# Optimization experiments

Hardware: AMD Instinct MI355X
Metric: run time of the kernel (lower is better)

## Reference

```python
import jax, jax.numpy as jnp
import numpy as np

SCALE = 1.0  # args.scale


def setup_inputs() -> dict:
    key = jax.random.key(0)
    k1, k2, k3, k4, k5 = jax.random.split(key, 5)
    B, S, D, R, LR = 4, 2048, 2048, 2048, 16  # batch, seq, column(emb), row(out), lora rank
    inp = jax.random.normal(k1, (B, S, D), dtype=jnp.float32)
    weight = jax.random.normal(k2, (R, D), dtype=jnp.float32) * (1.0 / np.sqrt(D))
    bias = jax.random.normal(k3, (R,), dtype=jnp.float32)
    lora_right = jax.random.normal(k4, (B, D, LR), dtype=jnp.float32) * 0.02
    lora_left = jax.random.normal(k5, (B, LR, R), dtype=jnp.float32) * 0.02
    return {"input": inp, "weight": weight, "bias": bias,
            "lora_right": lora_right, "lora_left": lora_left}


def reference(input, weight, bias, lora_right, lora_left):
    # Base linear: x @ W^T + b  -> [B, S, R]
    x = jnp.einsum('bsd,rd->bsr', input, weight) + bias
    # Per-sample low-rank LoRA chain: (input @ right) @ left, batched
    t = jnp.einsum('bsd,bdk->bsk', input, lora_right)   # [B, S, LR]
    y = jnp.einsum('bsk,bkr->bsr', t, lora_left)        # [B, S, R]
    # L2-normalize each token vector along the last dim, then scale
    y = y / jnp.linalg.norm(y, axis=-1, keepdims=True)
    y = y * SCALE
    return x + y
```

## Files before the change

### kernel.cpp

```cpp
#include <hip/hip_runtime.h>
#include <hip/hip_bf16.h>

#define SCALE_V 1.0f

typedef __bf16 bf16v8 __attribute__((ext_vector_type(8)));
typedef float f32v4 __attribute__((ext_vector_type(4)));

typedef const __attribute__((address_space(1))) void* gas_t;
typedef __attribute__((address_space(3))) void* las_t;
#define ASYNC_COPY16(g, l) \
    __builtin_amdgcn_global_load_lds((gas_t)(g), (las_t)(l), 16, 0, 0)
#define FENCE() asm volatile("" ::: "memory")
#define MFMA __builtin_amdgcn_mfma_f32_16x16x32_bf16

__global__ __launch_bounds__(256) void transpose_lr_kernel(
    const float* __restrict__ lright, __bf16* __restrict__ lrT) {
    __shared__ float tile[16][273];
    const int b = blockIdx.y;
    const int d0 = blockIdx.x * 256;
    const int t = threadIdx.x;
    const float* src = lright + (size_t)b * 32768 + (size_t)d0 * 16;
    #pragma unroll
    for (int j = 0; j < 16; ++j) {
        tile[t & 15][j * 16 + (t >> 4)] = src[j * 256 + t];
    }
    __syncthreads();
    const int k = t >> 4, dcol = t & 15;
    __bf16* dst = lrT + (size_t)b * 32768 + (size_t)k * 2048 + d0;
    #pragma unroll
    for (int j = 0; j < 16; ++j) {
        dst[dcol + j * 16] = (__bf16)tile[k][dcol + j * 16];
    }
}

__global__ __launch_bounds__(256) void prep_kernel(
    const float* __restrict__ inp, const float* __restrict__ wgt,
    const __bf16* __restrict__ lrT, const float* __restrict__ lleft,
    __bf16* __restrict__ abf, __bf16* __restrict__ wbf,
    float* __restrict__ tout, float* __restrict__ gpart) {
    __shared__ float sm[256];
    const int bid = blockIdx.x;
    const int tid = threadIdx.x;

    if (bid < 2048) {
        const int row0 = bid * 4;
        const int b = row0 >> 11;
        const __bf16* lt = lrT + (size_t)b * 32768;

        float x[4][8];
        #pragma unroll
        for (int rr = 0; rr < 4; ++rr) {
            const float* p = inp + (size_t)(row0 + rr) * 2048 + tid * 8;
            float4 a0 = *(const float4*)p;
            float4 a1 = *(const float4*)(p + 4);
            x[rr][0] = a0.x; x[rr][1] = a0.y; x[rr][2] = a0.z; x[rr][3] = a0.w;
            x[rr][4] = a1.x; x[rr][5] = a1.y; x[rr][6] = a1.z; x[rr][7] = a1.w;
            bf16v8 v;
            #pragma unroll
            for (int i = 0; i < 8; ++i) v[i] = (__bf16)x[rr][i];
            *(bf16v8*)(abf + (size_t)(row0 + rr) * 2048 + tid * 8) = v;
        }

        float v[64];
        #pragma unroll
        for (int k = 0; k < 16; ++k) {
            bf16v8 lb = *(const bf16v8*)(lt + (size_t)k * 2048 + tid * 8);
            float lv[8];
            #pragma unroll
            for (int i = 0; i < 8; ++i) lv[i] = (float)lb[i];
            #pragma unroll
            for (int rr = 0; rr < 4; ++rr) {
                float s = 0.f;
                #pragma unroll
                for (int i = 0; i < 8; ++i) s += x[rr][i] * lv[i];
                v[rr * 16 + k] = s;
            }
        }

        const int lane = tid & 63;
        const int w = tid >> 6;
        #pragma unroll
        for (int s = 1, cnt = 64; s < 64; s <<= 1, cnt >>= 1) {
            const int half = cnt >> 1;
            const bool up = (lane & s) != 0;
            #pragma unroll
            for (int i = 0; i < 32; ++i) {
                if (i < half) {
                    float keep = up ? v[i + half] : v[i];
                    float give = up ? v[i] : v[i + half];
                    v[i] = keep + __shfl_xor(give, s, 64);
                }
            }
        }
        const int rev = ((lane & 1) << 5) | ((lane & 2) << 3) | ((lane & 4) << 1) |
                        ((lane & 8) >> 1) | ((lane & 16) >> 3) | ((lane & 32) >> 5);
        sm[w * 64 + rev] = v[0];
        __syncthreads();
        if (tid < 64) {
            tout[(size_t)row0 * 16 + tid] =
                sm[tid] + sm[64 + tid] + sm[128 + tid] + sm[192 + tid];
        }
    } else if (bid < 4096) {
        const int i = ((bid - 2048) * 256 + tid) * 8;
        float4 x0 = *(const float4*)(wgt + i);
        float4 x1 = *(const float4*)(wgt + i + 4);
        bf16v8 v;
        v[0] = (__bf16)x0.x; v[1] = (__bf16)x0.y; v[2] = (__bf16)x0.z; v[3] = (__bf16)x0.w;
        v[4] = (__bf16)x1.x; v[5] = (__bf16)x1.y; v[6] = (__bf16)x1.z; v[7] = (__bf16)x1.w;
        *(bf16v8*)(wbf + i) = v;
    } else {
        const int g = bid - 4096;
        const int b = g >> 3, c = g & 7;
        const int k = tid >> 4, j = tid & 15;
        const float* pk = lleft + ((size_t)b * 16 + k) * 2048 + c * 256;
        const float* pj = lleft + ((size_t)b * 16 + j) * 2048 + c * 256;
        float s = 0.f;
        #pragma unroll 4
        for (int r = 0; r < 256; r += 4) {
            float4 a = *(const float4*)(pk + r);
            float4 d = *(const float4*)(pj + r);
            s += a.x * d.x + a.y * d.y + a.z * d.z + a.w * d.w;
        }
        gpart[((size_t)b * 8 + c) * 256 + tid] = s;
    }
}

__global__ __launch_bounds__(256) void norm_kernel(
    const float* __restrict__ gpart, float* __restrict__ t) {
    __shared__ float gs[256];
    const int tid = threadIdx.x;
    const int tok0 = blockIdx.x * 256;
    const int b = tok0 >> 11;
    float g = 0.f;
    #pragma unroll
    for (int c = 0; c < 8; ++c) g += gpart[((size_t)b * 8 + c) * 256 + tid];
    gs[tid] = g;
    __syncthreads();

    float* tp = t + (size_t)(tok0 + tid) * 16;
    float tv[16];
    {
        float4 a0 = *(const float4*)(tp);
        float4 a1 = *(const float4*)(tp + 4);
        float4 a2 = *(const float4*)(tp + 8);
        float4 a3 = *(const float4*)(tp + 12);
        tv[0]=a0.x; tv[1]=a0.y; tv[2]=a0.z; tv[3]=a0.w;
        tv[4]=a1.x; tv[5]=a1.y; tv[6]=a1.z; tv[7]=a1.w;
        tv[8]=a2.x; tv[9]=a2.y; tv[10]=a2.z; tv[11]=a2.w;
        tv[12]=a3.x; tv[13]=a3.y; tv[14]=a3.z; tv[15]=a3.w;
    }
    float q = 0.f;
    #pragma unroll
    for (int k = 0; k < 16; ++k) {
        float s = 0.f;
        #pragma unroll
        for (int j = 0; j < 16; ++j) s += gs[k * 16 + j] * tv[j];
        q += tv[k] * s;
    }
    const float r = SCALE_V * rsqrtf(q);
    float4 o;
    o.x = tv[0]*r;  o.y = tv[1]*r;  o.z = tv[2]*r;  o.w = tv[3]*r;  *(float4*)(tp)      = o;
    o.x = tv[4]*r;  o.y = tv[5]*r;  o.z = tv[6]*r;  o.w = tv[7]*r;  *(float4*)(tp + 4)  = o;
    o.x = tv[8]*r;  o.y = tv[9]*r;  o.z = tv[10]*r; o.w = tv[11]*r; *(float4*)(tp + 8)  = o;
    o.x = tv[12]*r; o.y = tv[13]*r; o.z = tv[14]*r; o.w = tv[15]*r; *(float4*)(tp + 12) = o;
}

__global__ __launch_bounds__(512, 2) void gemm_ep_kernel(
    const __bf16* __restrict__ abf, const __bf16* __restrict__ wbf,
    const float* __restrict__ bias, const float* __restrict__ tpr,
    const float* __restrict__ lleft, float* __restrict__ out) {
    __shared__ __attribute__((aligned(16))) char smem[131072];

    const int tid  = threadIdx.x;
    const int w    = tid >> 6;
    const int lane = tid & 63;
    const int l3   = lane >> 3, l7 = lane & 7;
    const int wm   = w >> 2;
    const int wn   = w & 3;
    const int fr   = lane & 15;

    const int xcd   = blockIdx.x & 7;
    const int local = blockIdx.x >> 3;
    const int tile_n = local & 7;
    const int tile_m = (xcd << 2) | (local >> 3);
    const int row0 = tile_m * 256;
    const int col0 = tile_n * 256;

    const int cswz = ((l7 ^ l3) * 8);
    const size_t aG0 = (size_t)(row0 + 8 * w + l3) * 2048 + cswz;
    const int bCh = 64 * (w >> 2) + 8 * (w & 3);
    const size_t bG0 = (size_t)(col0 + bCh + l3) * 2048 + cswz;
    char* const aDst = smem + 8 * w * 128 + lane * 16;
    char* const bDst = smem + 65536 + bCh * 128 + lane * 16;

#define STAGE_A(BUFOFF, S, KKEL)                                                         \
    do {                                                                                 \
        ASYNC_COPY16(abf + aG0 + (size_t)((S)*64) * 2048 + (KKEL),  aDst + (BUFOFF) + (S)*8192);          \
        ASYNC_COPY16(abf + aG0 + (size_t)((S)*64 + 128) * 2048 + (KKEL), aDst + (BUFOFF) + (S)*8192 + 16384); \
    } while (0)
#define STAGE_B(BUFOFF, S, KKEL)                                                         \
    do {                                                                                 \
        ASYNC_COPY16(wbf + bG0 + (size_t)((S)*32) * 2048 + (KKEL),  bDst + (BUFOFF) + (S)*4096);          \
        ASYNC_COPY16(wbf + bG0 + (size_t)((S)*32 + 128) * 2048 + (KKEL), bDst + (BUFOFF) + (S)*4096 + 16384); \
    } while (0)

    const int kx0 = (((lane >> 4) * 16) ^ (l7 << 4));
    const int kx1 = ((64 + (lane >> 4) * 16) ^ (l7 << 4));
    const char* const aRd = smem + (wm * 128 + fr) * 128;
    const char* const bRd = smem + 65536 + (wn * 64 + fr) * 128;

    f32v4 acc[8][4];
    #pragma unroll
    for (int m = 0; m < 8; ++m)
        #pragma unroll
        for (int n = 0; n < 4; ++n) {
            acc[m][n][0] = 0.f; acc[m][n][1] = 0.f;
            acc[m][n][2] = 0.f; acc[m][n][3] = 0.f;
        }

    STAGE_A(0, 0, 0);
    STAGE_B(0, 0, 0);
    STAGE_B(0, 1, 0);
    STAGE_A(0, 1, 0);
    STAGE_B(32768, 0, 64);
    STAGE_B(32768, 1, 64);
    STAGE_A(32768, 0, 64);
    asm volatile("s_waitcnt vmcnt(6)" ::: "memory");
    FENCE(); __builtin_amdgcn_s_barrier(); FENCE();

    for (int kt = 0; kt < 32; ++kt) {
        const int bo = (kt & 1) * 32768;
        const int bn = bo ^ 32768;
        const size_t kk1 = (size_t)((kt + 1) & 31) * 64;
        const size_t kk2 = (size_t)((kt + 2) & 31) * 64;
        bf16v8 af[4][2], bl[2][2], bh[2][2];

        #pragma unroll
        for (int m = 0; m < 4; ++m) {
            af[m][0] = *(const bf16v8*)(aRd + bo + m * 2048 + kx0);
            af[m][1] = *(const bf16v8*)(aRd + bo + m * 2048 + kx1);
        }
        #pragma unroll
        for (int n = 0; n < 2; ++n) {
            bl[n][0] = *(const bf16v8*)(bRd + bo + n * 2048 + kx0);
            bl[n][1] = *(const bf16v8*)(bRd + bo + n * 2048 + kx1);
        }
        STAGE_A(bn, 1, kk1);
        FENCE(); __builtin_amdgcn_s_barrier(); FENCE();
        __builtin_amdgcn_s_setprio(1);
        #pragma unroll
        for (int m = 0; m < 4; ++m)
            #pragma unroll
            for (int n = 0; n < 2; ++n) {
                acc[m][n] = MFMA(af[m][0], bl[n][0], acc[m][n], 0, 0, 0);
                acc[m][n] = MFMA(af[m][1], bl[n][1], acc[m][n], 0, 0, 0);
            }
        __builtin_amdgcn_s_setprio(0);
        FENCE(); __builtin_amdgcn_s_barrier(); FENCE();

        #pragma unroll
        for (int n = 0; n < 2; ++n) {
            bh[n][0] = *(const bf16v8*)(bRd + bo + (n + 2) * 2048 + kx0);
            bh[n][1] = *(const bf16v8*)(bRd + bo + (n + 2) * 2048 + kx1);
        }
        STAGE_B(bo, 0, kk2);
        FENCE(); __builtin_amdgcn_s_barrier(); FENCE();
        __builtin_amdgcn_s_setprio(1);
        #pragma unroll
        for (int m = 0; m < 4; ++m)
            #pragma unroll
            for (int n = 0; n < 2; ++n) {
                acc[m][n + 2] = MFMA(af[m][0], bh[n][0], acc[m][n + 2], 0, 0, 0);
                acc[m][n + 2] = MFMA(af[m][1], bh[n][1], acc[m][n + 2], 0, 0, 0);
            }
        __builtin_amdgcn_s_setprio(0);
        FENCE(); __builtin_amdgcn_s_barrier(); FENCE();

        #pragma unroll
        for (int m = 0; m < 4; ++m) {
            af[m][0] = *(const bf16v8*)(aRd + bo + (m + 4) * 2048 + kx0);
            af[m][1] = *(const bf16v8*)(aRd + bo + (m + 4) * 2048 + kx1);
        }
        STAGE_B(bo, 1, kk2);
        FENCE(); __builtin_amdgcn_s_barrier(); FENCE();
        __builtin_amdgcn_s_setprio(1);
        #pragma unroll
        for (int m = 0; m < 4; ++m)
            #pragma unroll
            for (int n = 0; n < 2; ++n) {
                acc[m + 4][n + 2] = MFMA(af[m][0], bh[n][0], acc[m + 4][n + 2], 0, 0, 0);
                acc[m + 4][n + 2] = MFMA(af[m][1], bh[n][1], acc[m + 4][n + 2], 0, 0, 0);
            }
        __builtin_amdgcn_s_setprio(0);
        FENCE(); __builtin_amdgcn_s_barrier(); FENCE();

        STAGE_A(bo, 0, kk2);
        asm volatile("s_waitcnt vmcnt(6)" ::: "memory");
        FENCE(); __builtin_amdgcn_s_barrier(); FENCE();
        __builtin_amdgcn_s_setprio(1);
        #pragma unroll
        for (int m = 0; m < 4; ++m)
            #pragma unroll
            for (int n = 0; n < 2; ++n) {
                acc[m + 4][n] = MFMA(af[m][0], bl[n][0], acc[m + 4][n], 0, 0, 0);
                acc[m + 4][n] = MFMA(af[m][1], bl[n][1], acc[m + 4][n], 0, 0, 0);
            }
        __builtin_amdgcn_s_setprio(0);
        FENCE(); __builtin_amdgcn_s_barrier(); FENCE();
    }

    asm volatile("s_waitcnt vmcnt(0)" ::: "memory");
    __syncthreads();
    {
        const int r = tid >> 1;
        const int h = (tid & 1) * 8;
        bf16v8 zv;
        #pragma unroll
        for (int i = 0; i < 8; ++i) zv[i] = (__bf16)0.f;

        __bf16* tE = (__bf16*)smem;
        __bf16* LE = (__bf16*)(smem + 20480);

        const float* tp = tpr + (size_t)(row0 + r) * 16 + h;
        float4 t0 = *(const float4*)tp;
        float4 t1 = *(const float4*)(tp + 4);
        bf16v8 tv;
        tv[0]=(__bf16)t0.x; tv[1]=(__bf16)t0.y; tv[2]=(__bf16)t0.z; tv[3]=(__bf16)t0.w;
        tv[4]=(__bf16)t1.x; tv[5]=(__bf16)t1.y; tv[6]=(__bf16)t1.z; tv[7]=(__bf16)t1.w;
        *(bf16v8*)(tE + r * 40 + h) = tv;
        *(bf16v8*)(tE + r * 40 + 16 + h) = zv;

        const int bb = row0 >> 11;
        const float* lp = lleft + ((size_t)bb * 16 + h) * 2048 + col0 + r;
        bf16v8 lv;
        #pragma unroll
        for (int i = 0; i < 8; ++i) lv[i] = (__bf16)lp[(size_t)i * 2048];
        *(bf16v8*)(LE + r * 40 + h) = lv;
        *(bf16v8*)(LE + r * 40 + 16 + h) = zv;
    }
    __syncthreads();
    {
        const __bf16* tE = (const __bf16*)smem;
        const __bf16* LE = (const __bf16*)(smem + 20480);
        const int ko = (lane >> 4) * 8;
        bf16v8 bE[4];
        #pragma unroll
        for (int n = 0; n < 4; ++n)
            bE[n] = *(const bf16v8*)(LE + (wn * 64 + n * 16 + fr) * 40 + ko);
        #pragma unroll
        for (int m = 0; m < 8; ++m) {
            bf16v8 aE = *(const bf16v8*)(tE + (wm * 128 + m * 16 + fr) * 40 + ko);
            #pragma unroll
            for (int n = 0; n < 4; ++n)
                acc[m][n] = MFMA(aE, bE[n], acc[m][n], 0, 0, 0);
        }
    }

    #pragma unroll
    for (int n = 0; n < 4; ++n) {
        const int gc = col0 + wn * 64 + n * 16 + fr;
        const float bv = bias[gc];
        #pragma unroll
        for (int m = 0; m < 8; ++m) {
            #pragma unroll
            for (int j = 0; j < 4; ++j) {
                const int gr = row0 + wm * 128 + m * 16 + (lane >> 4) * 4 + j;
                out[(size_t)gr * 2048 + gc] = acc[m][n][j] + bv;
            }
        }
    }
#undef STAGE_A
#undef STAGE_B
}

extern "C" void kernel_launch(void* const* d_in, const int* in_sizes, int n_in,
                              void* d_out, int out_size, void* d_ws, size_t ws_size,
                              hipStream_t stream) {
    const float* inp  = (const float*)d_in[0];
    const float* wgt  = (const float*)d_in[1];
    const float* bias = (const float*)d_in[2];
    const float* lrt  = (const float*)d_in[3];
    const float* llf  = (const float*)d_in[4];
    float* out = (float*)d_out;

    char* ws = (char*)d_ws;
    __bf16* abf  = (__bf16*)ws;
    __bf16* wbf  = (__bf16*)(ws + 33554432);
    float*  tbuf = (float*)(ws + 41943040);
    float*  gprt = (float*)(ws + 42467328);
    __bf16* lrT  = (__bf16*)(ws + 42500096);

    transpose_lr_kernel<<<dim3(8, 4), 256, 0, stream>>>(lrt, lrT);
    prep_kernel<<<4128, 256, 0, stream>>>(inp, wgt, lrT, llf, abf, wbf, tbuf, gprt);
    norm_kernel<<<32, 256, 0, stream>>>(gprt, tbuf);
    gemm_ep_kernel<<<dim3(256), 512, 0, stream>>>(abf, wbf, bias, tbuf, llf, out);
}
```

Baseline: 107.9 us.

## Fuse norm kernel into GEMM epilogue and prefetch B fragments across iterations

Removes the separate norm_kernel launch. Each GEMM block now reduces the Gram partials and normalizes its own 256 tokens' low-rank vectors in the epilogue before the correction MFMA. Separately, the low-half B fragment loads are moved to the end of the previous iteration, reading the next buffer, so they overlap the barrier. This saves a kernel launch and a round trip of the t buffer through global memory. The cost is that 256 blocks each redo the small 16x16 quadratic form for their rows, and the software-pipelined B loads add register pressure.

Measured after the change: 105.9 us. No clear change (-1.9%).

```diff
diff --git a/kernel.cpp b/kernel.cpp
--- a/kernel.cpp
+++ b/kernel.cpp
@@ -125,50 +125,11 @@
     }
 }
 
-__global__ __launch_bounds__(256) void norm_kernel(
-    const float* __restrict__ gpart, float* __restrict__ t) {
-    __shared__ float gs[256];
-    const int tid = threadIdx.x;
-    const int tok0 = blockIdx.x * 256;
-    const int b = tok0 >> 11;
-    float g = 0.f;
-    #pragma unroll
-    for (int c = 0; c < 8; ++c) g += gpart[((size_t)b * 8 + c) * 256 + tid];
-    gs[tid] = g;
-    __syncthreads();
-
-    float* tp = t + (size_t)(tok0 + tid) * 16;
-    float tv[16];
-    {
-        float4 a0 = *(const float4*)(tp);
-        float4 a1 = *(const float4*)(tp + 4);
-        float4 a2 = *(const float4*)(tp + 8);
-        float4 a3 = *(const float4*)(tp + 12);
-        tv[0]=a0.x; tv[1]=a0.y; tv[2]=a0.z; tv[3]=a0.w;
-        tv[4]=a1.x; tv[5]=a1.y; tv[6]=a1.z; tv[7]=a1.w;
-        tv[8]=a2.x; tv[9]=a2.y; tv[10]=a2.z; tv[11]=a2.w;
-        tv[12]=a3.x; tv[13]=a3.y; tv[14]=a3.z; tv[15]=a3.w;
-    }
-    float q = 0.f;
-    #pragma unroll
-    for (int k = 0; k < 16; ++k) {
-        float s = 0.f;
-        #pragma unroll
-        for (int j = 0; j < 16; ++j) s += gs[k * 16 + j] * tv[j];
-        q += tv[k] * s;
-    }
-    const float r = SCALE_V * rsqrtf(q);
-    float4 o;
-    o.x = tv[0]*r;  o.y = tv[1]*r;  o.z = tv[2]*r;  o.w = tv[3]*r;  *(float4*)(tp)      = o;
-    o.x = tv[4]*r;  o.y = tv[5]*r;  o.z = tv[6]*r;  o.w = tv[7]*r;  *(float4*)(tp + 4)  = o;
-    o.x = tv[8]*r;  o.y = tv[9]*r;  o.z = tv[10]*r; o.w = tv[11]*r; *(float4*)(tp + 8)  = o;
-    o.x = tv[12]*r; o.y = tv[13]*r; o.z = tv[14]*r; o.w = tv[15]*r; *(float4*)(tp + 12) = o;
-}
-
 __global__ __launch_bounds__(512, 2) void gemm_ep_kernel(
     const __bf16* __restrict__ abf, const __bf16* __restrict__ wbf,
-    const float* __restrict__ bias, const float* __restrict__ tpr,
-    const float* __restrict__ lleft, float* __restrict__ out) {
+    const float* __restrict__ bias, const float* __restrict__ traw,
+    const float* __restrict__ gpart, const float* __restrict__ lleft,
+    float* __restrict__ out) {
     __shared__ __attribute__((aligned(16))) char smem[131072];
 
     const int tid  = threadIdx.x;
@@ -228,23 +189,25 @@
     asm volatile("s_waitcnt vmcnt(6)" ::: "memory");
     FENCE(); __builtin_amdgcn_s_barrier(); FENCE();
 
+    bf16v8 bl[2][2];
+    #pragma unroll
+    for (int n = 0; n < 2; ++n) {
+        bl[n][0] = *(const bf16v8*)(bRd + n * 2048 + kx0);
+        bl[n][1] = *(const bf16v8*)(bRd + n * 2048 + kx1);
+    }
+
     for (int kt = 0; kt < 32; ++kt) {
         const int bo = (kt & 1) * 32768;
         const int bn = bo ^ 32768;
         const size_t kk1 = (size_t)((kt + 1) & 31) * 64;
         const size_t kk2 = (size_t)((kt + 2) & 31) * 64;
-        bf16v8 af[4][2], bl[2][2], bh[2][2];
+        bf16v8 af[4][2], bh[2][2];
 
         #pragma unroll
         for (int m = 0; m < 4; ++m) {
             af[m][0] = *(const bf16v8*)(aRd + bo + m * 2048 + kx0);
             af[m][1] = *(const bf16v8*)(aRd + bo + m * 2048 + kx1);
         }
-        #pragma unroll
-        for (int n = 0; n < 2; ++n) {
-            bl[n][0] = *(const bf16v8*)(bRd + bo + n * 2048 + kx0);
-            bl[n][1] = *(const bf16v8*)(bRd + bo + n * 2048 + kx1);
-        }
         STAGE_A(bn, 1, kk1);
         FENCE(); __builtin_amdgcn_s_barrier(); FENCE();
         __builtin_amdgcn_s_setprio(1);
@@ -306,39 +269,73 @@
                 acc[m + 4][n] = MFMA(af[m][1], bl[n][1], acc[m + 4][n], 0, 0, 0);
             }
         __builtin_amdgcn_s_setprio(0);
+        #pragma unroll
+        for (int n = 0; n < 2; ++n) {
+            bl[n][0] = *(const bf16v8*)(bRd + bn + n * 2048 + kx0);
+            bl[n][1] = *(const bf16v8*)(bRd + bn + n * 2048 + kx1);
+        }
         FENCE(); __builtin_amdgcn_s_barrier(); FENCE();
     }
 
     asm volatile("s_waitcnt vmcnt(0)" ::: "memory");
     __syncthreads();
     {
-        const int r = tid >> 1;
-        const int h = (tid & 1) * 8;
         bf16v8 zv;
         #pragma unroll
         for (int i = 0; i < 8; ++i) zv[i] = (__bf16)0.f;
 
-        __bf16* tE = (__bf16*)smem;
-        __bf16* LE = (__bf16*)(smem + 20480);
-
-        const float* tp = tpr + (size_t)(row0 + r) * 16 + h;
-        float4 t0 = *(const float4*)tp;
-        float4 t1 = *(const float4*)(tp + 4);
-        bf16v8 tv;
-        tv[0]=(__bf16)t0.x; tv[1]=(__bf16)t0.y; tv[2]=(__bf16)t0.z; tv[3]=(__bf16)t0.w;
-        tv[4]=(__bf16)t1.x; tv[5]=(__bf16)t1.y; tv[6]=(__bf16)t1.z; tv[7]=(__bf16)t1.w;
-        *(bf16v8*)(tE + r * 40 + h) = tv;
-        *(bf16v8*)(tE + r * 40 + 16 + h) = zv;
-
+        __bf16* tE  = (__bf16*)smem;
+        __bf16* LE  = (__bf16*)(smem + 20480);
+        float*  gsf = (float*)(smem + 40960);
         const int bb = row0 >> 11;
-        const float* lp = lleft + ((size_t)bb * 16 + h) * 2048 + col0 + r;
-        bf16v8 lv;
-        #pragma unroll
-        for (int i = 0; i < 8; ++i) lv[i] = (__bf16)lp[(size_t)i * 2048];
-        *(bf16v8*)(LE + r * 40 + h) = lv;
-        *(bf16v8*)(LE + r * 40 + 16 + h) = zv;
-    }
-    __syncthreads();
+
+        if (tid < 256) {
+            float g = 0.f;
+            #pragma unroll
+            for (int c = 0; c < 8; ++c) g += gpart[((size_t)bb * 8 + c) * 256 + tid];
+            gsf[tid] = g;
+        }
+        {
+            const int r = tid >> 1;
+            const int h = (tid & 1) * 8;
+            const float* lp = lleft + ((size_t)bb * 16 + h) * 2048 + col0 + r;
+            bf16v8 lv;
+            #pragma unroll
+            for (int i = 0; i < 8; ++i) lv[i] = (__bf16)lp[(size_t)i * 2048];
+            *(bf16v8*)(LE + r * 40 + h) = lv;
+            *(bf16v8*)(LE + r * 40 + 16 + h) = zv;
+        }
+        __syncthreads();
+        if (tid < 256) {
+            const float* tp = traw + (size_t)(row0 + tid) * 16;
+            float4 a0 = *(const float4*)(tp);
+            float4 a1 = *(const float4*)(tp + 4);
+            float4 a2 = *(const float4*)(tp + 8);
+            float4 a3 = *(const float4*)(tp + 12);
+            float tv[16] = {a0.x, a0.y, a0.z, a0.w, a1.x, a1.y, a1.z, a1.w,
+                            a2.x, a2.y, a2.z, a2.w, a3.x, a3.y, a3.z, a3.w};
+            float q = 0.f;
+            #pragma unroll
+            for (int k = 0; k < 16; ++k) {
+                float s = 0.f;
+                #pragma unroll
+                for (int j = 0; j < 16; ++j) s += gsf[k * 16 + j] * tv[j];
+                q += tv[k] * s;
+            }
+            const float sc = SCALE_V * rsqrtf(q);
+            bf16v8 t0v, t1v;
+            #pragma unroll
+            for (int i = 0; i < 8; ++i) {
+                t0v[i] = (__bf16)(tv[i] * sc);
+                t1v[i] = (__bf16)(tv[8 + i] * sc);
+            }
+            *(bf16v8*)(tE + tid * 40)      = t0v;
+            *(bf16v8*)(tE + tid * 40 + 8)  = t1v;
+            *(bf16v8*)(tE + tid * 40 + 16) = zv;
+            *(bf16v8*)(tE + tid * 40 + 24) = zv;
+        }
+        __syncthreads();
+    }
     {
         const __bf16* tE = (const __bf16*)smem;
         const __bf16* LE = (const __bf16*)(smem + 20480);
@@ -392,6 +389,5 @@
 
     transpose_lr_kernel<<<dim3(8, 4), 256, 0, stream>>>(lrt, lrT);
     prep_kernel<<<4128, 256, 0, stream>>>(inp, wgt, lrT, llf, abf, wbf, tbuf, gprt);
-    norm_kernel<<<32, 256, 0, stream>>>(gprt, tbuf);
-    gemm_ep_kernel<<<dim3(256), 512, 0, stream>>>(abf, wbf, bias, tbuf, llf, out);
+    gemm_ep_kernel<<<dim3(256), 512, 0, stream>>>(abf, wbf, bias, tbuf, gprt, llf, out);
 }
```
